# Optimization experiments

Hardware: AMD Instinct MI355X
Metric: run time of the kernel (lower is better)

The kernel has to match this reference:

```python
import jax, jax.numpy as jnp
import numpy as np

IGNORE_LABEL_ID = -100
GRID = 40                 # grid_width
PATH = 6                  # path_token_id
SP_W = 10.0               # spatial_penalty_weight
CONN_W = 5.0              # connectivity_weight
SEQ = GRID * GRID         # 1600
BIG = SEQ                 # sentinel larger than any flat index


def _spatial_penalty(pred):
    """Vectorized version of spatial_connectivity_loss's per-batch python loop.
    For each predicted path token, find the NEXT path token in flat order and
    penalize Manhattan jumps > 1. pred: [B, SEQ] int."""
    B = pred.shape[0]
    mask = pred == PATH                                   # [B,S]
    idx = jnp.arange(SEQ, dtype=jnp.int32)
    cand = jnp.where(mask, idx[None, :], BIG)
    # nxt[b,i] = smallest path index >= i (reverse cumulative min)
    nxt = jax.lax.cummin(cand, axis=1, reverse=True)
    # next path index strictly after i
    nxt_after = jnp.concatenate([nxt[:, 1:], jnp.full((B, 1), BIG, nxt.dtype)], axis=1)
    valid = mask & (nxt_after < BIG)                      # pairs (i, next)
    p2 = jnp.minimum(nxt_after, SEQ - 1)                  # keep indices in-range
    r1, c1 = idx // GRID, idx % GRID
    r2, c2 = p2 // GRID, p2 % GRID
    dist = jnp.abs(r1[None, :] - r2) + jnp.abs(c1[None, :] - c2)
    pen = jnp.where(valid & (dist > 1), (dist - 1).astype(jnp.float32) * SP_W, 0.0)
    return pen.sum() / B


def _connectivity_penalty(pred):
    """Parallel connected-component labeling (min-label propagation) replacing
    the CPU flood fill. pred: [B, SEQ] int."""
    B = pred.shape[0]
    mask = pred.reshape(B, GRID, GRID) == PATH
    idx = jnp.arange(SEQ, dtype=jnp.int32).reshape(GRID, GRID)
    lab0 = jnp.where(mask, idx[None], BIG)

    def prop(lab):
        p = jnp.pad(lab, ((0, 0), (1, 1), (1, 1)), constant_values=BIG)
        nmin = jnp.minimum(jnp.minimum(p[:, :-2, 1:-1], p[:, 2:, 1:-1]),
                           jnp.minimum(p[:, 1:-1, :-2], p[:, 1:-1, 2:]))
        return jnp.where(mask, jnp.minimum(lab, nmin), BIG)

    def cond(st):
        return st[1]

    def body(st):
        lab, _ = st
        new = prop(lab)
        return (new, jnp.any(new != lab))

    lab, _ = jax.lax.while_loop(cond, body, (lab0, jnp.array(True)))
    # a component is counted once at its minimal (root) cell
    comp = (mask & (lab == idx[None])).sum(axis=(1, 2))
    pen = jnp.where(comp > 1, (comp - 1).astype(jnp.float32) * CONN_W, 0.0)
    return pen.sum() / B


def setup_inputs() -> dict:
    key = jax.random.key(0)
    k1, k2, k3, k4, k5 = jax.random.split(key, 5)
    B, S, V = 1024, SEQ, 32
    return {
        "logits": jax.random.normal(k1, (B, S, V), dtype=jnp.float32),
        "labels": jax.random.randint(k2, (B, S), 0, V).astype(jnp.int64),
        "q_halt_logits": jax.random.normal(k3, (B,), dtype=jnp.float32),
        "halted": jax.random.randint(k4, (B,), 0, 2).astype(bool),
        "steps": jax.random.randint(k5, (B,), 0, 16).astype(jnp.int32),
    }


def reference(logits, labels, q_halt_logits, halted, steps):
    # halted/steps feed no-grad metrics only; loss math below matches ACTLossHead.
    mask = labels != IGNORE_LABEL_ID                       # [B,S]
    loss_counts = mask.sum(-1)
    loss_divisor = jnp.maximum(loss_counts, 1)[:, None].astype(logits.dtype)

    pred = jnp.argmax(logits, axis=-1)                     # [B,S]
    is_correct = mask & (pred == labels)
    seq_is_correct = is_correct.sum(-1) == loss_counts     # [B] bool

    # softmax cross entropy with ignore_index, per token
    logp = jax.nn.log_softmax(logits, axis=-1)
    safe_labels = jnp.maximum(labels, 0)
    ce = -jnp.take_along_axis(logp, safe_labels[..., None], axis=-1)[..., 0]
    ce = jnp.where(mask, ce, 0.0)
    lm_loss = (ce / loss_divisor).sum()

    # BCE-with-logits, reduction='sum'
    t = seq_is_correct.astype(logits.dtype)
    x = q_halt_logits
    q_halt_loss = (jnp.maximum(x, 0) - x * t + jnp.log1p(jnp.exp(-jnp.abs(x)))).sum()

    spatial_loss = _spatial_penalty(pred)
    connectivity_loss = _connectivity_penalty(pred)

    total_loss = lm_loss + 0.5 * q_halt_loss + spatial_loss + connectivity_loss
    return total_loss
```

## Files before the change

kernel.cpp:

```cpp
#include <hip/hip_runtime.h>
#include <cstdint>

#define GRIDW   40
#define SEQ     1600
#define NVOCAB  32
#define PATH_ID 6
#define IGNORE_ID (-100)
#define NWORDS  25
#define BLK     256
#define NWAVES  (BLK / 64)

__global__ __launch_bounds__(BLK) void act_loss_kernel(
    const float* __restrict__ logits,
    const int*   __restrict__ labels,
    const float* __restrict__ qhalt,
    float*       __restrict__ out,
    int B)
{
    const int b    = blockIdx.x;
    const int tid  = threadIdx.x;
    const int lane = tid & 63;
    const int wid  = tid >> 6;
    const int sub  = tid & 7;

    __shared__ uint8_t  path[SEQ];
    __shared__ uint16_t lab[SEQ];
    __shared__ uint16_t pos[SEQ];
    __shared__ uint64_t words[NWORDS];
    __shared__ int      offs[NWORDS + 1];
    __shared__ int      npath_s;
    __shared__ float    wr_f[NWAVES];
    __shared__ int      wr_i[NWAVES];
    __shared__ int      wr_j[NWAVES];
    __shared__ float    part_a;

    float ce_sum = 0.0f;
    int   cnt = 0, cor = 0;

    const float* base  = logits + (size_t)b * SEQ * NVOCAB;
    const int*   lbase = labels + (size_t)b * SEQ;

    const int tokOff = tid >> 3;
    for (int i0 = 0; i0 < SEQ; i0 += BLK / 8) {
        const int tok = i0 + tokOff;
        float4 v = ((const float4*)(base + (size_t)tok * NVOCAB))[sub];
        int lbl = lbase[tok];

        float m = v.x;
        if (v.y > m) m = v.y;
        if (v.z > m) m = v.z;
        if (v.w > m) m = v.w;
        for (int d = 1; d < 8; d <<= 1)
            m = fmaxf(m, __shfl_xor(m, d));
        int cand = 999;
        if (v.w == m) cand = 4 * sub + 3;
        if (v.z == m) cand = 4 * sub + 2;
        if (v.y == m) cand = 4 * sub + 1;
        if (v.x == m) cand = 4 * sub + 0;
        for (int d = 1; d < 8; d <<= 1)
            cand = min(cand, __shfl_xor(cand, d));

        float s = __expf(v.x - m) + __expf(v.y - m)
                + __expf(v.z - m) + __expf(v.w - m);
        for (int d = 1; d < 8; d <<= 1)
            s += __shfl_xor(s, d);

        bool msk  = (lbl != IGNORE_ID);
        int  slbl = (lbl < 0) ? 0 : lbl;
        int   k2    = slbl & 3;
        float xcand = (k2 == 0) ? v.x : (k2 == 1) ? v.y : (k2 == 2) ? v.z : v.w;
        int   owner = (lane & ~7) | ((slbl >> 2) & 7);
        float xl    = __shfl(xcand, owner);

        if (sub == 0) {
            float lse = m + __logf(s);
            ce_sum += msk ? (lse - xl) : 0.0f;
            cnt    += msk ? 1 : 0;
            cor    += (msk && cand == lbl) ? 1 : 0;
            path[tok] = (cand == PATH_ID) ? 1 : 0;
        }
    }
    __syncthreads();

    for (int basei = 0; basei < SEQ; basei += BLK) {
        int idx = basei + tid;
        bool p = (idx < SEQ) ? (path[idx] != 0) : false;
        uint64_t w = __ballot(p);
        int widx = (basei >> 6) + wid;
        if (lane == 0 && widx < NWORDS) words[widx] = w;
    }

    for (int d = 1; d < 64; d <<= 1) {
        ce_sum += __shfl_xor(ce_sum, d);
        cnt    += __shfl_xor(cnt, d);
        cor    += __shfl_xor(cor, d);
    }
    if (lane == 0) { wr_f[wid] = ce_sum; wr_i[wid] = cnt; wr_j[wid] = cor; }
    __syncthreads();

    if (tid == 0) {
        float ce_tot = wr_f[0] + wr_f[1] + wr_f[2] + wr_f[3];
        int   c_tot  = wr_i[0] + wr_i[1] + wr_i[2] + wr_i[3];
        int   k_tot  = wr_j[0] + wr_j[1] + wr_j[2] + wr_j[3];
        float lm = ce_tot / (float)max(c_tot, 1);
        float t  = (k_tot == c_tot) ? 1.0f : 0.0f;
        float xq = qhalt[b];
        float bce = fmaxf(xq, 0.0f) - xq * t + log1pf(expf(-fabsf(xq)));
        part_a = lm + 0.5f * bce;
    }

    if (wid == 0) {
        uint64_t w = (lane < NWORDS) ? words[lane] : 0ull;
        int pc = __popcll(w);
        int c = pc;
        for (int d = 1; d < 32; d <<= 1) {
            int t = __shfl_up(c, d);
            if (lane >= d) c += t;
        }
        if (lane < NWORDS) offs[lane] = c - pc;
        if (lane == NWORDS - 1) { offs[NWORDS] = c; npath_s = c; }
    }
    __syncthreads();

    if (tid < NWORDS) {
        int o = offs[tid];
        uint64_t w = words[tid];
        int basei = tid * 64;
        while (w) {
            int k = __ffsll((unsigned long long)w) - 1;
            pos[o++] = (uint16_t)(basei + k);
            w &= (w - 1);
        }
    }
    __syncthreads();

    const int np = npath_s;
    int sp_units = 0;
    for (int q = tid; q + 1 < np; q += BLK) {
        int i = pos[q], j = pos[q + 1];
        int dist = abs(i / GRIDW - j / GRIDW) + abs(i % GRIDW - j % GRIDW);
        if (dist > 1) sp_units += dist - 1;
    }

    for (int i = tid; i < SEQ; i += BLK)
        lab[i] = path[i] ? (uint16_t)i : (uint16_t)0xFFFF;
    __syncthreads();

    for (;;) {
        int local = 0;
        for (int i = tid; i < SEQ; i += BLK) {
            if (!path[i]) continue;
            int r = i / GRIDW, c = i % GRIDW;
            uint16_t v = lab[i];
            uint16_t nm = v;
            if (r > 0)         { uint16_t u = lab[i - GRIDW]; nm = (u < nm) ? u : nm; }
            if (r < GRIDW - 1) { uint16_t u = lab[i + GRIDW]; nm = (u < nm) ? u : nm; }
            if (c > 0)         { uint16_t u = lab[i - 1];     nm = (u < nm) ? u : nm; }
            if (c < GRIDW - 1) { uint16_t u = lab[i + 1];     nm = (u < nm) ? u : nm; }
            if (nm < v) { lab[i] = nm; local = 1; }
        }
        if (__syncthreads_count(local) == 0) break;
    }

    int comp = 0;
    for (int i = tid; i < SEQ; i += BLK)
        comp += (path[i] && lab[i] == (uint16_t)i) ? 1 : 0;

    for (int d = 1; d < 64; d <<= 1) {
        sp_units += __shfl_xor(sp_units, d);
        comp     += __shfl_xor(comp, d);
    }
    if (lane == 0) { wr_i[wid] = sp_units; wr_j[wid] = comp; }
    __syncthreads();

    if (tid == 0) {
        int sp_tot   = wr_i[0] + wr_i[1] + wr_i[2] + wr_i[3];
        int comp_tot = wr_j[0] + wr_j[1] + wr_j[2] + wr_j[3];
        int conn_units = (comp_tot > 1) ? (comp_tot - 1) : 0;
        float total = part_a +
                      ((float)sp_tot * 10.0f + (float)conn_units * 5.0f) / (float)B;
        atomicAdd(out, total);
    }
}

extern "C" void kernel_launch(void* const* d_in, const int* in_sizes, int n_in,
                              void* d_out, int out_size, void* d_ws, size_t ws_size,
                              hipStream_t stream) {
    const float* logits = (const float*)d_in[0];
    const int*   labels = (const int*)d_in[1];
    const float* qhalt  = (const float*)d_in[2];
    float* out = (float*)d_out;
    const int B = in_sizes[2];

    hipMemsetAsync(out, 0, (size_t)out_size * sizeof(float), stream);
    act_loss_kernel<<<dim3(B), dim3(BLK), 0, stream>>>(logits, labels, qhalt, out, B);
}
```

Baseline: 326.5 us.

## Stage logits through padded LDS tiles so each lane owns one token row

The first pass no longer spreads each token across 8 lanes with shuffle reductions. Each wave now loads 64 tokens' logits with coalesced float4 loads and transposes them through a padded per-wave LDS tile, so every lane processes one full 32-wide row serially. Max, argmax, sum-exp and the label logit lookup then run in registers and LDS without cross-lane shuffles. The lab and pos arrays alias the staging buffer to keep shared memory use in check. The cost is a larger LDS footprint, which may reduce occupancy, plus extra LDS write and read traffic, and the argmax tie-breaking is now done per lane.

```diff
diff --git a/kernel.cpp b/kernel.cpp
--- a/kernel.cpp
+++ b/kernel.cpp
@@ -9,6 +9,7 @@
 #define NWORDS  25
 #define BLK     256
 #define NWAVES  (BLK / 64)
+#define TILE_F4 576
 
 __global__ __launch_bounds__(BLK) void act_loss_kernel(
     const float* __restrict__ logits,
@@ -21,11 +22,9 @@
     const int tid  = threadIdx.x;
     const int lane = tid & 63;
     const int wid  = tid >> 6;
-    const int sub  = tid & 7;
-
+
+    __shared__ __align__(16) float4 stage4[NWAVES * TILE_F4];
     __shared__ uint8_t  path[SEQ];
-    __shared__ uint16_t lab[SEQ];
-    __shared__ uint16_t pos[SEQ];
     __shared__ uint64_t words[NWORDS];
     __shared__ int      offs[NWORDS + 1];
     __shared__ int      npath_s;
@@ -34,51 +33,66 @@
     __shared__ int      wr_j[NWAVES];
     __shared__ float    part_a;
 
+    uint16_t* lab = (uint16_t*)stage4;
+    uint16_t* pos = (uint16_t*)stage4 + SEQ;
+
     float ce_sum = 0.0f;
     int   cnt = 0, cor = 0;
 
-    const float* base  = logits + (size_t)b * SEQ * NVOCAB;
-    const int*   lbase = labels + (size_t)b * SEQ;
-
-    const int tokOff = tid >> 3;
-    for (int i0 = 0; i0 < SEQ; i0 += BLK / 8) {
-        const int tok = i0 + tokOff;
-        float4 v = ((const float4*)(base + (size_t)tok * NVOCAB))[sub];
+    const float4* gbase = (const float4*)(logits + (size_t)b * SEQ * NVOCAB);
+    const int*    lbase = labels + (size_t)b * SEQ;
+
+    float4* stg  = stage4 + wid * TILE_F4;
+    const float* frow_base = (const float*)stg;
+
+    for (int t = wid; t < SEQ / 64; t += NWAVES) {
+        const float4* gp = gbase + (size_t)t * 512;
+
+        float4 g[8];
+#pragma unroll
+        for (int k = 0; k < 8; ++k)
+            g[k] = gp[k * 64 + lane];
+
+        int tok = t * 64 + lane;
         int lbl = lbase[tok];
 
-        float m = v.x;
-        if (v.y > m) m = v.y;
-        if (v.z > m) m = v.z;
-        if (v.w > m) m = v.w;
-        for (int d = 1; d < 8; d <<= 1)
-            m = fmaxf(m, __shfl_xor(m, d));
-        int cand = 999;
-        if (v.w == m) cand = 4 * sub + 3;
-        if (v.z == m) cand = 4 * sub + 2;
-        if (v.y == m) cand = 4 * sub + 1;
-        if (v.x == m) cand = 4 * sub + 0;
-        for (int d = 1; d < 8; d <<= 1)
-            cand = min(cand, __shfl_xor(cand, d));
-
-        float s = __expf(v.x - m) + __expf(v.y - m)
-                + __expf(v.z - m) + __expf(v.w - m);
-        for (int d = 1; d < 8; d <<= 1)
-            s += __shfl_xor(s, d);
+#pragma unroll
+        for (int k = 0; k < 8; ++k)
+            stg[(k * 8 + (lane >> 3)) * 9 + (lane & 7)] = g[k];
+
+        float4 x[8];
+#pragma unroll
+        for (int j = 0; j < 8; ++j)
+            x[j] = stg[lane * 9 + j];
+
+        float m = x[0].x; int arg = 0;
+#pragma unroll
+        for (int j = 0; j < 8; ++j) {
+            int i4 = 4 * j;
+            if (j > 0 && x[j].x > m) { m = x[j].x; arg = i4; }
+            if (x[j].y > m) { m = x[j].y; arg = i4 + 1; }
+            if (x[j].z > m) { m = x[j].z; arg = i4 + 2; }
+            if (x[j].w > m) { m = x[j].w; arg = i4 + 3; }
+        }
+        float s0 = 0.f, s1 = 0.f, s2 = 0.f, s3 = 0.f;
+#pragma unroll
+        for (int j = 0; j < 8; ++j) {
+            s0 += __expf(x[j].x - m);
+            s1 += __expf(x[j].y - m);
+            s2 += __expf(x[j].z - m);
+            s3 += __expf(x[j].w - m);
+        }
+        float s = (s0 + s1) + (s2 + s3);
 
         bool msk  = (lbl != IGNORE_ID);
         int  slbl = (lbl < 0) ? 0 : lbl;
-        int   k2    = slbl & 3;
-        float xcand = (k2 == 0) ? v.x : (k2 == 1) ? v.y : (k2 == 2) ? v.z : v.w;
-        int   owner = (lane & ~7) | ((slbl >> 2) & 7);
-        float xl    = __shfl(xcand, owner);
-
-        if (sub == 0) {
-            float lse = m + __logf(s);
-            ce_sum += msk ? (lse - xl) : 0.0f;
-            cnt    += msk ? 1 : 0;
-            cor    += (msk && cand == lbl) ? 1 : 0;
-            path[tok] = (cand == PATH_ID) ? 1 : 0;
-        }
+        float xl = frow_base[lane * 36 + slbl];
+
+        float lse = m + __logf(s);
+        ce_sum += msk ? (lse - xl) : 0.0f;
+        cnt    += msk ? 1 : 0;
+        cor    += (msk && arg == lbl) ? 1 : 0;
+        path[tok] = (arg == PATH_ID) ? 1 : 0;
     }
     __syncthreads();
 
```

After: 307.7 us. 5.8% less time.

## Process one token per thread with online softmax and double block size

Applied to the files above, without the earlier changes.

Each thread now handles a whole token: it loads all 32 logits as eight float4s and computes argmax, log-sum-exp and the label logit with an online max/rescale. This replaces the earlier scheme of 8 lanes per token with shuffle reductions. The path ballot is folded into the main loop, the label initialisation moves earlier so one barrier can be dropped, and the block grows to 512 threads with a launch-bounds occupancy hint. The aim is to remove cross-lane shuffle traffic and extra passes and barriers. The trade-offs are per-lane strided 128-byte loads instead of coalesced ones, higher register pressure, and an uneven last iteration, since 1600 tokens do not divide evenly into 512 threads.

```diff
diff --git a/kernel.cpp b/kernel.cpp
--- a/kernel.cpp
+++ b/kernel.cpp
@@ -7,10 +7,10 @@
 #define PATH_ID 6
 #define IGNORE_ID (-100)
 #define NWORDS  25
-#define BLK     256
+#define BLK     512
 #define NWAVES  (BLK / 64)
 
-__global__ __launch_bounds__(BLK) void act_loss_kernel(
+__global__ __launch_bounds__(BLK, 8) void act_loss_kernel(
     const float* __restrict__ logits,
     const int*   __restrict__ labels,
     const float* __restrict__ qhalt,
@@ -21,7 +21,6 @@
     const int tid  = threadIdx.x;
     const int lane = tid & 63;
     const int wid  = tid >> 6;
-    const int sub  = tid & 7;
 
     __shared__ uint8_t  path[SEQ];
     __shared__ uint16_t lab[SEQ];
@@ -40,55 +39,58 @@
     const float* base  = logits + (size_t)b * SEQ * NVOCAB;
     const int*   lbase = labels + (size_t)b * SEQ;
 
-    const int tokOff = tid >> 3;
-    for (int i0 = 0; i0 < SEQ; i0 += BLK / 8) {
-        const int tok = i0 + tokOff;
-        float4 v = ((const float4*)(base + (size_t)tok * NVOCAB))[sub];
-        int lbl = lbase[tok];
-
-        float m = v.x;
-        if (v.y > m) m = v.y;
-        if (v.z > m) m = v.z;
-        if (v.w > m) m = v.w;
-        for (int d = 1; d < 8; d <<= 1)
-            m = fmaxf(m, __shfl_xor(m, d));
-        int cand = 999;
-        if (v.w == m) cand = 4 * sub + 3;
-        if (v.z == m) cand = 4 * sub + 2;
-        if (v.y == m) cand = 4 * sub + 1;
-        if (v.x == m) cand = 4 * sub + 0;
-        for (int d = 1; d < 8; d <<= 1)
-            cand = min(cand, __shfl_xor(cand, d));
-
-        float s = __expf(v.x - m) + __expf(v.y - m)
-                + __expf(v.z - m) + __expf(v.w - m);
-        for (int d = 1; d < 8; d <<= 1)
-            s += __shfl_xor(s, d);
-
-        bool msk  = (lbl != IGNORE_ID);
-        int  slbl = (lbl < 0) ? 0 : lbl;
-        int   k2    = slbl & 3;
-        float xcand = (k2 == 0) ? v.x : (k2 == 1) ? v.y : (k2 == 2) ? v.z : v.w;
-        int   owner = (lane & ~7) | ((slbl >> 2) & 7);
-        float xl    = __shfl(xcand, owner);
-
-        if (sub == 0) {
-            float lse = m + __logf(s);
-            ce_sum += msk ? (lse - xl) : 0.0f;
-            cnt    += msk ? 1 : 0;
-            cor    += (msk && cand == lbl) ? 1 : 0;
-            path[tok] = (cand == PATH_ID) ? 1 : 0;
-        }
-    }
-    __syncthreads();
-
-    for (int basei = 0; basei < SEQ; basei += BLK) {
-        int idx = basei + tid;
-        bool p = (idx < SEQ) ? (path[idx] != 0) : false;
-        uint64_t w = __ballot(p);
-        int widx = (basei >> 6) + wid;
-        if (lane == 0 && widx < NWORDS) words[widx] = w;
-    }
+#define CH(qa, qb, b0)                                                      \
+    {                                                                       \
+        float cm = qa.x; int ca = (b0);                                     \
+        if (qa.y > cm) { cm = qa.y; ca = (b0) + 1; }                        \
+        if (qa.z > cm) { cm = qa.z; ca = (b0) + 2; }                        \
+        if (qa.w > cm) { cm = qa.w; ca = (b0) + 3; }                        \
+        if (qb.x > cm) { cm = qb.x; ca = (b0) + 4; }                        \
+        if (qb.y > cm) { cm = qb.y; ca = (b0) + 5; }                        \
+        if (qb.z > cm) { cm = qb.z; ca = (b0) + 6; }                        \
+        if (qb.w > cm) { cm = qb.w; ca = (b0) + 7; }                        \
+        if ((b0) == 0) { m = cm; arg = ca; }                                \
+        else if (cm > m) { s *= __expf(m - cm); m = cm; arg = ca; }         \
+        s += __expf(qa.x - m) + __expf(qa.y - m)                            \
+           + __expf(qa.z - m) + __expf(qa.w - m)                            \
+           + __expf(qb.x - m) + __expf(qb.y - m)                            \
+           + __expf(qb.z - m) + __expf(qb.w - m);                           \
+        if ((slbl >> 3) == ((b0) >> 3)) {                                   \
+            int k = slbl & 7;                                               \
+            xl = (k == 0) ? qa.x : (k == 1) ? qa.y : (k == 2) ? qa.z :      \
+                 (k == 3) ? qa.w : (k == 4) ? qb.x : (k == 5) ? qb.y :      \
+                 (k == 6) ? qb.z : qb.w;                                    \
+        }                                                                   \
+    }
+
+#pragma unroll 1
+    for (int i = tid; i < SEQ; i += BLK) {
+        const float4* p4 = (const float4*)(base + (size_t)i * NVOCAB);
+        float4 q0 = p4[0], q1 = p4[1], q2 = p4[2], q3 = p4[3];
+        float4 q4 = p4[4], q5 = p4[5], q6 = p4[6], q7 = p4[7];
+        int lbl  = lbase[i];
+        int slbl = (lbl < 0) ? 0 : lbl;
+
+        float m, xl = 0.0f, s = 0.0f;
+        int   arg;
+        CH(q0, q1, 0)
+        CH(q2, q3, 8)
+        CH(q4, q5, 16)
+        CH(q6, q7, 24)
+
+        bool msk = (lbl != IGNORE_ID);
+        float lse = m + __logf(s);
+        ce_sum += msk ? (lse - xl) : 0.0f;
+        cnt    += msk ? 1 : 0;
+        cor    += (msk && arg == lbl) ? 1 : 0;
+
+        bool pf = (arg == PATH_ID);
+        path[i] = pf ? 1 : 0;
+        uint64_t w = __ballot(pf);
+        if (lane == 0) words[i >> 6] = w;
+    }
+#undef CH
+    __syncthreads();
 
     for (int d = 1; d < 64; d <<= 1) {
         ce_sum += __shfl_xor(ce_sum, d);
@@ -99,9 +101,11 @@
     __syncthreads();
 
     if (tid == 0) {
-        float ce_tot = wr_f[0] + wr_f[1] + wr_f[2] + wr_f[3];
-        int   c_tot  = wr_i[0] + wr_i[1] + wr_i[2] + wr_i[3];
-        int   k_tot  = wr_j[0] + wr_j[1] + wr_j[2] + wr_j[3];
+        float ce_tot = 0.0f; int c_tot = 0, k_tot = 0;
+#pragma unroll
+        for (int v = 0; v < NWAVES; ++v) {
+            ce_tot += wr_f[v]; c_tot += wr_i[v]; k_tot += wr_j[v];
+        }
         float lm = ce_tot / (float)max(c_tot, 1);
         float t  = (k_tot == c_tot) ? 1.0f : 0.0f;
         float xq = qhalt[b];
@@ -122,6 +126,8 @@
     }
     __syncthreads();
 
+    for (int i = tid; i < SEQ; i += BLK)
+        lab[i] = path[i] ? (uint16_t)i : (uint16_t)0xFFFF;
     if (tid < NWORDS) {
         int o = offs[tid];
         uint64_t w = words[tid];
@@ -141,10 +147,6 @@
         int dist = abs(i / GRIDW - j / GRIDW) + abs(i % GRIDW - j % GRIDW);
         if (dist > 1) sp_units += dist - 1;
     }
-
-    for (int i = tid; i < SEQ; i += BLK)
-        lab[i] = path[i] ? (uint16_t)i : (uint16_t)0xFFFF;
-    __syncthreads();
 
     for (;;) {
         int local = 0;
@@ -174,8 +176,9 @@
     __syncthreads();
 
     if (tid == 0) {
-        int sp_tot   = wr_i[0] + wr_i[1] + wr_i[2] + wr_i[3];
-        int comp_tot = wr_j[0] + wr_j[1] + wr_j[2] + wr_j[3];
+        int sp_tot = 0, comp_tot = 0;
+#pragma unroll
+        for (int v = 0; v < NWAVES; ++v) { sp_tot += wr_i[v]; comp_tot += wr_j[v]; }
         int conn_units = (comp_tot > 1) ? (comp_tot - 1) : 0;
         float total = part_a +
                       ((float)sp_tot * 10.0f + (float)conn_units * 5.0f) / (float)B;
```

Result: faster. 303.3 us (-7.1%).
